# Kernel tuning notes

Hardware: AMD Instinct MI355X
Metric: run time of the kernel (lower is better)

The kernel has to match this reference:

```python
import jax, jax.numpy as jnp
import numpy as np

N = 100000   # nodes
E = 1000000  # edges
D = 128      # hidden dim (all n_hidden entries)
ED = 21      # edge_dim hard-coded in the module


def setup_inputs() -> dict:
    key = jax.random.key(0)
    ks = jax.random.split(key, 32)
    w = lambda k, shape: (jax.random.normal(k, shape, dtype=jnp.float32) * 0.05)
    inp = {
        "G": jax.random.normal(ks[0], (N, D), dtype=jnp.float32),
        "edge_index": jax.random.randint(ks[1], (2, E), 0, N),
        "edge_attribute": jax.random.normal(ks[2], (E, ED), dtype=jnp.float32),
        # 3-layer node embedding MLP (stacked since all dims are D)
        "emb_W": w(ks[3], (3, D, D)), "emb_b": w(ks[4], (3, D)),
        # 2 ResGatedGraphConv layers (conv3 is unused in forward)
        "key_W": w(ks[5], (2, D, D)), "key_b": w(ks[6], (2, D)),
        "qry_W": w(ks[7], (2, D, D)), "qry_b": w(ks[8], (2, D)),
        "val_W": w(ks[9], (2, D, D)), "val_b": w(ks[10], (2, D)),
        "skp_W": w(ks[11], (2, D, D)), "skp_b": w(ks[12], (2, D)),
        "edg_W": w(ks[13], (2, ED, D)), "edg_b": w(ks[14], (2, D)),
        # graph linears
        "g1_W": w(ks[15], (D, D)), "g1_b": w(ks[16], (D,)),
        "g2_W": w(ks[17], (D, D)), "g2_b": w(ks[18], (D,)),
        # head: concat(node, graph_mean) -> 2D -> D -> D -> 1
        "h1_W": w(ks[19], (2 * D, D)), "h1_b": w(ks[20], (D,)),
        "h2_W": w(ks[21], (D, D)), "h2_b": w(ks[22], (D,)),
        "h3_W": w(ks[23], (D, 1)), "h3_b": w(ks[24], (1,)),
    }
    return inp


def reference(G, edge_index, edge_attribute,
              emb_W, emb_b, key_W, key_b, qry_W, qry_b, val_W, val_b,
              skp_W, skp_b, edg_W, edg_b,
              g1_W, g1_b, g2_W, g2_b, h1_W, h1_b, h2_W, h2_b, h3_W, h3_b):
    x = G
    # embedding MLP: Linear -> ReLU x3
    for i in range(3):
        x = jax.nn.relu(x @ emb_W[i] + emb_b[i])
    src, dst = edge_index[0], edge_index[1]
    # ResGatedGraphConv (PyG): out_i = W_skip x_i + sum_j sigmoid(k_i + q_j + W_e e_ij) * v_j
    for i in range(2):
        k = x @ key_W[i] + key_b[i]   # per target node i
        q = x @ qry_W[i] + qry_b[i]   # per source node j
        v = x @ val_W[i] + val_b[i]
        eta = jax.nn.sigmoid(k[dst] + q[src] + edge_attribute @ edg_W[i] + edg_b[i])  # [E, D]
        agg = jax.ops.segment_sum(eta * v[src], dst, num_segments=N)  # scatter-add [N, D]
        x = jax.nn.relu(agg + x @ skp_W[i] + skp_b[i])
    x = jax.nn.relu(x @ g1_W + g1_b)
    x = x @ g2_W + g2_b
    # per-node concat with mean-pooled graph embedding (vectorized form of the Python loop)
    gmean = jnp.mean(x, axis=0)
    u = jnp.concatenate([x, jnp.broadcast_to(gmean, x.shape)], axis=-1)  # [N, 2D]
    u = jax.nn.relu(u @ h1_W + h1_b)
    u = jax.nn.relu(u @ h2_W + h2_b)
    return u @ h3_W + h3_b  # [N, 1]
```

## Files before the change

kernel.cpp:

```cpp
#include <hip/hip_runtime.h>
#include <hip/hip_bf16.h>

#define DD 128
#define LW 136

typedef __attribute__((ext_vector_type(8))) short bf16x8;
typedef __attribute__((ext_vector_type(4))) float f32x4;

__device__ __forceinline__ void cvt8(const float4 a0, const float4 a1,
                                     bf16x8& hi, bf16x8& lo)
{
    float af[8] = {a0.x, a0.y, a0.z, a0.w, a1.x, a1.y, a1.z, a1.w};
    union { unsigned int u[4]; bf16x8 v; } H, L;
    #pragma unroll
    for (int i = 0; i < 4; ++i) {
        unsigned int b0 = __float_as_uint(af[2*i]);
        unsigned int b1 = __float_as_uint(af[2*i+1]);
        unsigned int h0 = b0 & 0xFFFF0000u;
        unsigned int h1 = b1 & 0xFFFF0000u;
        H.u[i] = (h0 >> 16) | h1;
        float r0 = af[2*i]   - __uint_as_float(h0);
        float r1 = af[2*i+1] - __uint_as_float(h1);
        L.u[i] = (__float_as_uint(r0) >> 16) | (__float_as_uint(r1) & 0xFFFF0000u);
    }
    hi = H.v; lo = L.v;
}

__device__ __forceinline__ float fsig(float z)
{
    return __builtin_amdgcn_rcpf(1.f + __expf(-z));
}

__device__ __forceinline__ void mfma_step(
    const unsigned short* __restrict__ WH, const unsigned short* __restrict__ WL,
    int wavecol, int l15, int kb,
    const bf16x8 ah[4], const bf16x8 al[4], f32x4 acc[4][2])
{
    bf16x8 bh[2], bl[2];
    #pragma unroll
    for (int ni = 0; ni < 2; ++ni) {
        int m = wavecol + ni * 16 + l15;
        bh[ni] = *(const bf16x8*)(WH + (size_t)m * DD + kb);
        bl[ni] = *(const bf16x8*)(WL + (size_t)m * DD + kb);
    }
    #pragma unroll
    for (int mi = 0; mi < 4; ++mi)
        #pragma unroll
        for (int ni = 0; ni < 2; ++ni) {
            acc[mi][ni] = __builtin_amdgcn_mfma_f32_16x16x32_bf16(ah[mi], bh[ni], acc[mi][ni], 0, 0, 0);
            acc[mi][ni] = __builtin_amdgcn_mfma_f32_16x16x32_bf16(ah[mi], bl[ni], acc[mi][ni], 0, 0, 0);
            acc[mi][ni] = __builtin_amdgcn_mfma_f32_16x16x32_bf16(al[mi], bh[ni], acc[mi][ni], 0, 0, 0);
        }
}

__device__ __forceinline__ void glb_layer(
    const float* __restrict__ X, int ldX, const int arow[4],
    const unsigned short* __restrict__ WU,
    int wavecol, int l15, int kg, f32x4 acc[4][2])
{
    const unsigned short* WH = WU;
    const unsigned short* WL = WU + 16384;
    #pragma unroll
    for (int kc = 0; kc < 4; ++kc) {
        const int kb = kc * 32 + kg;
        bf16x8 ah[4], al[4];
        #pragma unroll
        for (int mi = 0; mi < 4; ++mi) {
            const float* p = X + (size_t)arow[mi] * ldX + kb;
            float4 a0 = *(const float4*)p;
            float4 a1 = *(const float4*)(p + 4);
            cvt8(a0, a1, ah[mi], al[mi]);
        }
        mfma_step(WH, WL, wavecol, l15, kb, ah, al, acc);
    }
}

__device__ __forceinline__ void lds_layer(
    const unsigned short (*AH)[LW], const unsigned short (*AL)[LW],
    const unsigned short* __restrict__ WU,
    int wavecol, int l15, int kg, f32x4 acc[4][2])
{
    const unsigned short* WH = WU;
    const unsigned short* WL = WU + 16384;
    #pragma unroll
    for (int kc = 0; kc < 4; ++kc) {
        const int kb = kc * 32 + kg;
        bf16x8 ah[4], al[4];
        #pragma unroll
        for (int mi = 0; mi < 4; ++mi) {
            ah[mi] = *(const bf16x8*)&AH[mi * 16 + l15][kb];
            al[mi] = *(const bf16x8*)&AL[mi * 16 + l15][kb];
        }
        mfma_step(WH, WL, wavecol, l15, kb, ah, al, acc);
    }
}

__device__ __forceinline__ void epi_lds(
    const f32x4 acc[4][2], unsigned short (*AH)[LW], unsigned short (*AL)[LW],
    const float* __restrict__ bias, int wavecol, int l15, int rg, int relu)
{
    #pragma unroll
    for (int ni = 0; ni < 2; ++ni) {
        const int col = wavecol + ni * 16 + l15;
        const float bv = bias[col];
        #pragma unroll
        for (int mi = 0; mi < 4; ++mi)
            #pragma unroll
            for (int r = 0; r < 4; ++r) {
                const int row = mi * 16 + rg + r;
                float v = acc[mi][ni][r] + bv;
                if (relu) v = fmaxf(v, 0.f);
                unsigned int u = __float_as_uint(v), h = u & 0xFFFF0000u;
                float res = v - __uint_as_float(h);
                AH[row][col] = (unsigned short)(h >> 16);
                AL[row][col] = (unsigned short)(__float_as_uint(res) >> 16);
            }
    }
}

__global__ __launch_bounds__(256) void fused_emb3q(
    const float* __restrict__ G, const unsigned short* __restrict__ Wt,
    const float* __restrict__ embb, const float* __restrict__ biasCat,
    float* __restrict__ bfused, int N)
{
    __shared__ unsigned short AH[64][LW], AL[64][LW];
    const int lane = threadIdx.x & 63, wid = threadIdx.x >> 6;
    const int wavecol = wid * 32;
    const int l15 = lane & 15, kg = (lane >> 4) * 8, rg = (lane >> 4) * 4;
    const int row0 = blockIdx.x * 64;

    int arow[4];
    #pragma unroll
    for (int mi = 0; mi < 4; ++mi) {
        int r = row0 + mi * 16 + l15;
        arow[mi] = r < N ? r : N - 1;
    }

    f32x4 acc[4][2] = {};
    glb_layer(G, DD, arow, Wt, wavecol, l15, kg, acc);
    epi_lds(acc, AH, AL, embb, wavecol, l15, rg, 1);
    __syncthreads();

    #pragma unroll
    for (int mi = 0; mi < 4; ++mi)
        #pragma unroll
        for (int ni = 0; ni < 2; ++ni) acc[mi][ni] = (f32x4){0,0,0,0};
    lds_layer(AH, AL, Wt + 32768, wavecol, l15, kg, acc);
    __syncthreads();
    epi_lds(acc, AH, AL, embb + 128, wavecol, l15, rg, 1);
    __syncthreads();

    #pragma unroll
    for (int mi = 0; mi < 4; ++mi)
        #pragma unroll
        for (int ni = 0; ni < 2; ++ni) acc[mi][ni] = (f32x4){0,0,0,0};
    lds_layer(AH, AL, Wt + 65536, wavecol, l15, kg, acc);
    __syncthreads();
    epi_lds(acc, AH, AL, embb + 256, wavecol, l15, rg, 1);
    __syncthreads();

    for (int cb = 0; cb < 4; ++cb) {
        #pragma unroll
        for (int mi = 0; mi < 4; ++mi)
            #pragma unroll
            for (int ni = 0; ni < 2; ++ni) acc[mi][ni] = (f32x4){0,0,0,0};
        lds_layer(AH, AL, Wt + (size_t)(3 + cb) * 32768, wavecol, l15, kg, acc);
        #pragma unroll
        for (int ni = 0; ni < 2; ++ni) {
            const int gcol = cb * 128 + wavecol + ni * 16 + l15;
            const float bv = biasCat[gcol];
            #pragma unroll
            for (int mi = 0; mi < 4; ++mi)
                #pragma unroll
                for (int r = 0; r < 4; ++r) {
                    int row = row0 + mi * 16 + rg + r;
                    if (row < N)
                        bfused[(size_t)row * 512 + gcol] = acc[mi][ni][r] + bv;
                }
        }
    }
}

__global__ __launch_bounds__(256) void fused_kqvs(
    float* __restrict__ bfused, const unsigned short* __restrict__ Wt,
    const float* __restrict__ biasCat, int N)
{
    __shared__ unsigned short AH[64][LW], AL[64][LW];
    const int tid = threadIdx.x;
    const int lane = tid & 63, wid = tid >> 6;
    const int wavecol = wid * 32;
    const int l15 = lane & 15, kg = (lane >> 4) * 8, rg = (lane >> 4) * 4;
    const int row0 = blockIdx.x * 64;

    for (int idx = tid; idx < 64 * 128; idx += 256) {
        const int row = idx >> 7, col = idx & 127;
        int gr = row0 + row; if (gr >= N) gr = N - 1;
        float v = bfused[(size_t)gr * 512 + col];
        unsigned int u = __float_as_uint(v), h = u & 0xFFFF0000u;
        float res = v - __uint_as_float(h);
        AH[row][col] = (unsigned short)(h >> 16);
        AL[row][col] = (unsigned short)(__float_as_uint(res) >> 16);
    }
    __syncthreads();

    f32x4 acc[4][2];
    for (int cb = 0; cb < 4; ++cb) {
        #pragma unroll
        for (int mi = 0; mi < 4; ++mi)
            #pragma unroll
            for (int ni = 0; ni < 2; ++ni) acc[mi][ni] = (f32x4){0,0,0,0};
        lds_layer(AH, AL, Wt + (size_t)cb * 32768, wavecol, l15, kg, acc);
        #pragma unroll
        for (int ni = 0; ni < 2; ++ni) {
            const int gcol = cb * 128 + wavecol + ni * 16 + l15;
            const float bv = biasCat[gcol];
            #pragma unroll
            for (int mi = 0; mi < 4; ++mi)
                #pragma unroll
                for (int r = 0; r < 4; ++r) {
                    int row = row0 + mi * 16 + rg + r;
                    if (row < N)
                        bfused[(size_t)row * 512 + gcol] = acc[mi][ni][r] + bv;
                }
        }
    }
}

__global__ __launch_bounds__(256) void fused_g12(
    float* __restrict__ bfused, const unsigned short* __restrict__ Wt,
    const float* __restrict__ g1b, const float* __restrict__ g2b,
    float* __restrict__ gsum, int N)
{
    __shared__ unsigned short AH[64][LW], AL[64][LW];
    __shared__ float csum[128];
    const int tid = threadIdx.x;
    const int lane = tid & 63, wid = tid >> 6;
    const int wavecol = wid * 32;
    const int l15 = lane & 15, kg = (lane >> 4) * 8, rg = (lane >> 4) * 4;
    const int row0 = blockIdx.x * 64;

    if (tid < 128) csum[tid] = 0.f;

    int arow[4];
    #pragma unroll
    for (int mi = 0; mi < 4; ++mi) {
        int r = row0 + mi * 16 + l15;
        arow[mi] = r < N ? r : N - 1;
    }

    f32x4 acc[4][2] = {};
    glb_layer(bfused, 512, arow, Wt, wavecol, l15, kg, acc);
    epi_lds(acc, AH, AL, g1b, wavecol, l15, rg, 1);
    __syncthreads();

    #pragma unroll
    for (int mi = 0; mi < 4; ++mi)
        #pragma unroll
        for (int ni = 0; ni < 2; ++ni) acc[mi][ni] = (f32x4){0,0,0,0};
    lds_layer(AH, AL, Wt + 32768, wavecol, l15, kg, acc);

    #pragma unroll
    for (int ni = 0; ni < 2; ++ni) {
        const int col = wavecol + ni * 16 + l15;
        const float bv = g2b[col];
        float part = 0.f;
        #pragma unroll
        for (int mi = 0; mi < 4; ++mi)
            #pragma unroll
            for (int r = 0; r < 4; ++r) {
                int row = row0 + mi * 16 + rg + r;
                if (row < N) {
                    float v = acc[mi][ni][r] + bv;
                    bfused[(size_t)row * 512 + 128 + col] = v;
                    part += v;
                }
            }
        atomicAdd(&csum[col], part);
    }
    __syncthreads();
    if (tid < 128) atomicAdd(&gsum[tid], csum[tid]);
}

__global__ __launch_bounds__(256) void fused_head(
    const float* __restrict__ bfused, const unsigned short* __restrict__ Wt,
    const float* __restrict__ cvec, const float* __restrict__ h2b,
    const float* __restrict__ h3w, const float* __restrict__ h3b,
    float* __restrict__ out, int N)
{
    __shared__ unsigned short AH[64][LW], AL[64][LW];
    const int tid = threadIdx.x;
    const int lane = tid & 63, wid = tid >> 6;
    const int wavecol = wid * 32;
    const int l15 = lane & 15, kg = (lane >> 4) * 8, rg = (lane >> 4) * 4;
    const int row0 = blockIdx.x * 64;

    int arow[4];
    #pragma unroll
    for (int mi = 0; mi < 4; ++mi) {
        int r = row0 + mi * 16 + l15;
        arow[mi] = r < N ? r : N - 1;
    }

    f32x4 acc[4][2] = {};
    glb_layer(bfused + 128, 512, arow, Wt, wavecol, l15, kg, acc);
    epi_lds(acc, AH, AL, cvec, wavecol, l15, rg, 1);
    __syncthreads();

    #pragma unroll
    for (int mi = 0; mi < 4; ++mi)
        #pragma unroll
        for (int ni = 0; ni < 2; ++ni) acc[mi][ni] = (f32x4){0,0,0,0};
    lds_layer(AH, AL, Wt + 32768, wavecol, l15, kg, acc);
    __syncthreads();
    epi_lds(acc, AH, AL, h2b, wavecol, l15, rg, 1);
    __syncthreads();

    const int row = tid >> 2, seg = tid & 3;
    float s = 0.f;
    #pragma unroll 8
    for (int j = 0; j < 32; ++j) {
        int col = seg * 32 + j;
        float xv = __uint_as_float((unsigned int)AH[row][col] << 16)
                 + __uint_as_float((unsigned int)AL[row][col] << 16);
        s = fmaf(xv, h3w[col], s);
    }
    s += __shfl_xor(s, 1, 64);
    s += __shfl_xor(s, 2, 64);
    if (seg == 0 && row0 + row < N) out[row0 + row] = s + h3b[0];
}

__global__ __launch_bounds__(256) void prep_weights(
    const float* __restrict__ embW, const float* __restrict__ keyW,
    const float* __restrict__ qryW, const float* __restrict__ valW,
    const float* __restrict__ skpW, const float* __restrict__ g1W,
    const float* __restrict__ g2W, const float* __restrict__ h1W,
    const float* __restrict__ h2W,
    const float* __restrict__ keyb, const float* __restrict__ qryb,
    const float* __restrict__ valb, const float* __restrict__ skpb,
    unsigned short* __restrict__ Wt, float* __restrict__ biasCat)
{
    const int u = blockIdx.x;
    const int t = threadIdx.x;
    __shared__ float T[128][129];

    const float* src;
    if (u < 3)       src = embW + (size_t)u * 16384;
    else if (u < 7)  { const float* p[4] = {keyW, qryW, valW, skpW}; src = p[u - 3]; }
    else if (u < 11) { const float* p[4] = {keyW, qryW, valW, skpW}; src = p[u - 7] + 16384; }
    else if (u == 11) src = g1W;
    else if (u == 12) src = g2W;
    else if (u == 13) src = h1W;
    else              src = h2W;

    #pragma unroll
    for (int i = 0; i < 64; ++i) {
        int idx = t + 256 * i;
        T[idx >> 7][idx & 127] = src[idx];
    }
    __syncthreads();

    unsigned short* dH = Wt + (size_t)u * 32768;
    unsigned short* dL = dH + 16384;
    const int m = t >> 1, kbase = (t & 1) * 64;
    for (int j = 0; j < 64; ++j) {
        int k = kbase + j;
        float a = T[k][m];
        unsigned int b = __float_as_uint(a);
        unsigned int h = b & 0xFFFF0000u;
        float r = a - __uint_as_float(h);
        dH[m * 128 + k] = (unsigned short)(h >> 16);
        dL[m * 128 + k] = (unsigned short)(__float_as_uint(r) >> 16);
    }

    if (u == 0) {
        for (int x = t; x < 1024; x += 256) {
            int L = x >> 9, c = x & 511;
            const float* bp = (c < 128) ? keyb : (c < 256) ? qryb : (c < 384) ? valb : skpb;
            biasCat[x] = bp[L * 128 + (c & 127)];
        }
    }
}

__global__ void hist_kernel(const int* __restrict__ dstA, int* __restrict__ hist, int E)
{
    for (int e = blockIdx.x * blockDim.x + threadIdx.x; e < E;
         e += gridDim.x * blockDim.x)
        atomicAdd(&hist[dstA[e]], 1);
}

__global__ __launch_bounds__(256) void scan1_kernel(
    const int* __restrict__ in, int n_in,
    int* __restrict__ out, int* __restrict__ bsum, int n)
{
    __shared__ int wtot[4];
    const int t = threadIdx.x, lane = t & 63, wv = t >> 6;
    const int base = blockIdx.x * 1024 + t * 4;
    int v[4]; int sum = 0;
    #pragma unroll
    for (int j = 0; j < 4; ++j) {
        int idx = base + j;
        v[j] = (idx < n_in) ? in[idx] : 0;
        sum += v[j];
    }
    int incl = sum;
    #pragma unroll
    for (int d = 1; d < 64; d <<= 1) {
        int y = __shfl_up(incl, d, 64);
        if (lane >= d) incl += y;
    }
    if (lane == 63) wtot[wv] = incl;
    __syncthreads();
    int woff = 0;
    for (int w = 0; w < wv; ++w) woff += wtot[w];
    int run = woff + incl - sum;
    #pragma unroll
    for (int j = 0; j < 4; ++j) {
        int idx = base + j;
        if (idx < n) out[idx] = run;
        run += v[j];
    }
    if (t == 0)
        bsum[blockIdx.x] = wtot[0] + wtot[1] + wtot[2] + wtot[3];
}

__global__ void scan2_kernel(int* __restrict__ bsum, int nb)
{
    if (blockIdx.x == 0 && threadIdx.x == 0) {
        int run = 0;
        for (int i = 0; i < nb; ++i) { int t = bsum[i]; bsum[i] = run; run += t; }
    }
}

__global__ __launch_bounds__(256) void scan3_kernel(
    int* __restrict__ out, const int* __restrict__ bsum,
    int* __restrict__ cursor, int n, int n_nodes)
{
    const int base = blockIdx.x * 1024 + threadIdx.x * 4;
    const int add = bsum[blockIdx.x];
    #pragma unroll
    for (int j = 0; j < 4; ++j) {
        int idx = base + j;
        if (idx < n) {
            int vv = out[idx] + add;
            out[idx] = vv;
            if (idx < n_nodes) cursor[idx] = vv;
        }
    }
}

__global__ void scatter_ea(const int* __restrict__ srcA, const int* __restrict__ dstA,
                           const float* __restrict__ ea, int* __restrict__ cursor,
                           int* __restrict__ srcp, float* __restrict__ eaP, int E)
{
    for (int e = blockIdx.x * blockDim.x + threadIdx.x; e < E;
         e += gridDim.x * blockDim.x) {
        int d = dstA[e];
        int pos = atomicAdd(&cursor[d], 1);
        srcp[pos] = srcA[e];
        const float* s = ea + (size_t)e * 21;
        float* q = eaP + (size_t)pos * 24;
        #pragma unroll
        for (int j = 0; j < 21; ++j) q[j] = s[j];
    }
}

__global__ __launch_bounds__(256) void edge_agg16(
    const int* __restrict__ row_ptr, const int* __restrict__ srcp,
    const float* __restrict__ eaP,
    const float* __restrict__ We, const float* __restrict__ be,
    float* __restrict__ fused, int N)
{
    const int wv = threadIdx.x >> 6, lane = threadIdx.x & 63;
    const int c = lane * 2;

    float2 w[21];
    #pragma unroll
    for (int j = 0; j < 21; ++j)
        w[j] = *(const float2*)(We + j * DD + c);
    const float2 b2 = *(const float2*)(be + c);

    const int dstride = gridDim.x * 4;

    for (int d = blockIdx.x * 4 + wv; d < N; d += dstride) {
        const float2 kd = *(const float2*)(fused + (size_t)d * 512 + c);
        const float2 sk = *(const float2*)(fused + (size_t)d * 512 + 384 + c);

        float ax = 0.f, ay = 0.f;
        const int i0 = __builtin_amdgcn_readfirstlane(row_ptr[d]);
        const int i1 = __builtin_amdgcn_readfirstlane(row_ptr[d + 1]);

        for (int i = i0; i < i1; i += 2) {
            const int iA = i;
            const int iB = (i + 1 < i1) ? i + 1 : i1 - 1;
            const float wgtB = (i + 1 < i1) ? 1.f : 0.f;

            const int sA = __builtin_amdgcn_readfirstlane(srcp[iA]);
            const int sB = __builtin_amdgcn_readfirstlane(srcp[iB]);

            const float* eA = eaP + (size_t)iA * 24;
            const float* eB = eaP + (size_t)iB * 24;
            float aA[21], aB[21];
            #pragma unroll
            for (int j = 0; j < 21; ++j) { aA[j] = eA[j]; aB[j] = eB[j]; }

            const float* fpA = fused + (size_t)sA * 512;
            const float* fpB = fused + (size_t)sB * 512;
            float2 qA = *(const float2*)(fpA + 128 + c);
            float2 vA = *(const float2*)(fpA + 256 + c);
            float2 qB = *(const float2*)(fpB + 128 + c);
            float2 vB = *(const float2*)(fpB + 256 + c);

            float pxA[4] = {0,0,0,0}, pyA[4] = {0,0,0,0};
            float pxB[4] = {0,0,0,0}, pyB[4] = {0,0,0,0};
            #pragma unroll
            for (int j = 0; j < 21; ++j) {
                int s = j & 3;
                pxA[s] = fmaf(aA[j], w[j].x, pxA[s]);
                pyA[s] = fmaf(aA[j], w[j].y, pyA[s]);
                pxB[s] = fmaf(aB[j], w[j].x, pxB[s]);
                pyB[s] = fmaf(aB[j], w[j].y, pyB[s]);
            }
            float exA = (pxA[0] + pxA[1]) + (pxA[2] + pxA[3]) + b2.x;
            float eyA = (pyA[0] + pyA[1]) + (pyA[2] + pyA[3]) + b2.y;
            float exB = (pxB[0] + pxB[1]) + (pxB[2] + pxB[3]) + b2.x;
            float eyB = (pyB[0] + pyB[1]) + (pyB[2] + pyB[3]) + b2.y;

            float gxA = fsig(kd.x + qA.x + exA);
            float gyA = fsig(kd.y + qA.y + eyA);
            float gxB = wgtB * fsig(kd.x + qB.x + exB);
            float gyB = wgtB * fsig(kd.y + qB.y + eyB);

            ax = fmaf(gxA, vA.x, ax);
            ay = fmaf(gyA, vA.y, ay);
            ax = fmaf(gxB, vB.x, ax);
            ay = fmaf(gyB, vB.y, ay);
        }

        float* xr = fused + (size_t)d * 512;
        xr[c]     = fmaxf(ax + sk.x, 0.f);
        xr[c + 1] = fmaxf(ay + sk.y, 0.f);
    }
}

__global__ void cvec_kernel(const float* __restrict__ gsum, const float* __restrict__ h1W,
                            const float* __restrict__ h1b, float* __restrict__ cvec, float invN)
{
    const int m = threadIdx.x;
    float acc = h1b[m];
    for (int k = 0; k < 128; ++k)
        acc = fmaf(gsum[k] * invN, h1W[(size_t)(128 + k) * DD + m], acc);
    cvec[m] = acc;
}

extern "C" void kernel_launch(void* const* d_in, const int* in_sizes, int n_in,
                              void* d_out, int out_size, void* d_ws, size_t ws_size,
                              hipStream_t stream)
{
    const float* G    = (const float*)d_in[0];
    const int*   ei   = (const int*)  d_in[1];
    const float* ea   = (const float*)d_in[2];
    const float* embW = (const float*)d_in[3];
    const float* embb = (const float*)d_in[4];
    const float* keyW = (const float*)d_in[5];
    const float* keyb = (const float*)d_in[6];
    const float* qryW = (const float*)d_in[7];
    const float* qryb = (const float*)d_in[8];
    const float* valW = (const float*)d_in[9];
    const float* valb = (const float*)d_in[10];
    const float* skpW = (const float*)d_in[11];
    const float* skpb = (const float*)d_in[12];
    const float* edgW = (const float*)d_in[13];
    const float* edgb = (const float*)d_in[14];
    const float* g1W  = (const float*)d_in[15];
    const float* g1b  = (const float*)d_in[16];
    const float* g2W  = (const float*)d_in[17];
    const float* g2b  = (const float*)d_in[18];
    const float* h1W  = (const float*)d_in[19];
    const float* h1b  = (const float*)d_in[20];
    const float* h2W  = (const float*)d_in[21];
    const float* h2b  = (const float*)d_in[22];
    const float* h3W  = (const float*)d_in[23];
    const float* h3b  = (const float*)d_in[24];

    const int N = in_sizes[0] / DD;
    const int E = in_sizes[2] / 21;
    const int* srcA = ei;
    const int* dstA = ei + E;

    float* bfused = (float*)d_ws;
    float* gsum   = bfused + (size_t)N * 512;
    float* cvec   = gsum + DD;
    float* biasCat= cvec + DD;
    unsigned short* Wt = (unsigned short*)(biasCat + 1024);
    int* hist = (int*)((char*)Wt + (size_t)15 * 32768 * 2);
    int* row  = hist + N;
    int* cur  = row + N + 1;
    int* bsum = cur + N;
    int* srcp = bsum + 128;
    float* eaP = (float*)(srcp + E);

    const int fgrid   = (N + 63) / 64;
    const int aggGrid = 2048;
    const int nScan = N + 1;
    const int nb = (nScan + 1023) / 1024;

    prep_weights<<<15, 256, 0, stream>>>(embW, keyW, qryW, valW, skpW,
                                         g1W, g2W, h1W, h2W,
                                         keyb, qryb, valb, skpb, Wt, biasCat);
    hipMemsetAsync(hist, 0, (size_t)N * sizeof(int), stream);
    hipMemsetAsync(gsum, 0, DD * sizeof(float), stream);
    hist_kernel<<<1024, 256, 0, stream>>>(dstA, hist, E);
    scan1_kernel<<<nb, 256, 0, stream>>>(hist, N, row, bsum, nScan);
    scan2_kernel<<<1, 64, 0, stream>>>(bsum, nb);
    scan3_kernel<<<nb, 256, 0, stream>>>(row, bsum, cur, nScan, N);
    scatter_ea<<<1024, 256, 0, stream>>>(srcA, dstA, ea, cur, srcp, eaP, E);

    #define UNIT(u) (Wt + (size_t)(u) * 32768)

    fused_emb3q<<<fgrid, 256, 0, stream>>>(G, Wt, embb, biasCat, bfused, N);

    edge_agg16<<<aggGrid, 256, 0, stream>>>(row, srcp, eaP,
                                            edgW + 0, edgb + 0, bfused, N);

    fused_kqvs<<<fgrid, 256, 0, stream>>>(bfused, UNIT(7), biasCat + 512, N);
    edge_agg16<<<aggGrid, 256, 0, stream>>>(row, srcp, eaP,
                                            edgW + 21*DD, edgb + DD, bfused, N);

    fused_g12<<<fgrid, 256, 0, stream>>>(bfused, UNIT(11), g1b, g2b, gsum, N);

    cvec_kernel<<<1, DD, 0, stream>>>(gsum, h1W, h1b, cvec, 1.0f / (float)N);

    fused_head<<<fgrid, 256, 0, stream>>>(bfused, UNIT(13), cvec, h2b, h3W, h3b,
                                          (float*)d_out, N);
}
```

Measured before the change: 1.077 ms.

## Process two destination nodes per wavefront with one-shot grid instead of grid-stride

The edge aggregation kernel now assigns two destination nodes to each wavefront and walks their edge lists in lockstep, so the two independent gathers per iteration come from different nodes instead of consecutive edges of one node. The persistent grid-stride loop is replaced by a grid sized to cover all nodes once. This aims to improve memory-level parallelism and remove the odd-degree padding waste of the old pairing. The cost is imbalance when the two nodes' degrees differ, since the loop runs to the larger degree with masked work, and it pays the per-block weight load many more times.

```diff
diff --git a/kernel.cpp b/kernel.cpp
--- a/kernel.cpp
+++ b/kernel.cpp
@@ -464,13 +464,17 @@
     }
 }
 
-__global__ __launch_bounds__(256) void edge_agg16(
+__global__ __launch_bounds__(256) void edge_agg17(
     const int* __restrict__ row_ptr, const int* __restrict__ srcp,
     const float* __restrict__ eaP,
     const float* __restrict__ We, const float* __restrict__ be,
     float* __restrict__ fused, int N)
 {
     const int wv = threadIdx.x >> 6, lane = threadIdx.x & 63;
+    const int d0 = blockIdx.x * 8 + wv * 2;
+    const int d1 = d0 + 1;
+    if (d0 >= N) return;
+    const bool has1 = d1 < N;
     const int c = lane * 2;
 
     float2 w[21];
@@ -479,66 +483,78 @@
         w[j] = *(const float2*)(We + j * DD + c);
     const float2 b2 = *(const float2*)(be + c);
 
-    const int dstride = gridDim.x * 4;
-
-    for (int d = blockIdx.x * 4 + wv; d < N; d += dstride) {
-        const float2 kd = *(const float2*)(fused + (size_t)d * 512 + c);
-        const float2 sk = *(const float2*)(fused + (size_t)d * 512 + 384 + c);
-
-        float ax = 0.f, ay = 0.f;
-        const int i0 = __builtin_amdgcn_readfirstlane(row_ptr[d]);
-        const int i1 = __builtin_amdgcn_readfirstlane(row_ptr[d + 1]);
-
-        for (int i = i0; i < i1; i += 2) {
-            const int iA = i;
-            const int iB = (i + 1 < i1) ? i + 1 : i1 - 1;
-            const float wgtB = (i + 1 < i1) ? 1.f : 0.f;
-
-            const int sA = __builtin_amdgcn_readfirstlane(srcp[iA]);
-            const int sB = __builtin_amdgcn_readfirstlane(srcp[iB]);
-
-            const float* eA = eaP + (size_t)iA * 24;
-            const float* eB = eaP + (size_t)iB * 24;
-            float aA[21], aB[21];
-            #pragma unroll
-            for (int j = 0; j < 21; ++j) { aA[j] = eA[j]; aB[j] = eB[j]; }
-
-            const float* fpA = fused + (size_t)sA * 512;
-            const float* fpB = fused + (size_t)sB * 512;
-            float2 qA = *(const float2*)(fpA + 128 + c);
-            float2 vA = *(const float2*)(fpA + 256 + c);
-            float2 qB = *(const float2*)(fpB + 128 + c);
-            float2 vB = *(const float2*)(fpB + 256 + c);
-
-            float pxA[4] = {0,0,0,0}, pyA[4] = {0,0,0,0};
-            float pxB[4] = {0,0,0,0}, pyB[4] = {0,0,0,0};
-            #pragma unroll
-            for (int j = 0; j < 21; ++j) {
-                int s = j & 3;
-                pxA[s] = fmaf(aA[j], w[j].x, pxA[s]);
-                pyA[s] = fmaf(aA[j], w[j].y, pyA[s]);
-                pxB[s] = fmaf(aB[j], w[j].x, pxB[s]);
-                pyB[s] = fmaf(aB[j], w[j].y, pyB[s]);
-            }
-            float exA = (pxA[0] + pxA[1]) + (pxA[2] + pxA[3]) + b2.x;
-            float eyA = (pyA[0] + pyA[1]) + (pyA[2] + pyA[3]) + b2.y;
-            float exB = (pxB[0] + pxB[1]) + (pxB[2] + pxB[3]) + b2.x;
-            float eyB = (pyB[0] + pyB[1]) + (pyB[2] + pyB[3]) + b2.y;
-
-            float gxA = fsig(kd.x + qA.x + exA);
-            float gyA = fsig(kd.y + qA.y + eyA);
-            float gxB = wgtB * fsig(kd.x + qB.x + exB);
-            float gyB = wgtB * fsig(kd.y + qB.y + eyB);
-
-            ax = fmaf(gxA, vA.x, ax);
-            ay = fmaf(gyA, vA.y, ay);
-            ax = fmaf(gxB, vB.x, ax);
-            ay = fmaf(gyB, vB.y, ay);
-        }
-
-        float* xr = fused + (size_t)d * 512;
-        xr[c]     = fmaxf(ax + sk.x, 0.f);
-        xr[c + 1] = fmaxf(ay + sk.y, 0.f);
+    const float2 kd0 = *(const float2*)(fused + (size_t)d0 * 512 + c);
+    const float2 sk0 = *(const float2*)(fused + (size_t)d0 * 512 + 384 + c);
+    const float2 kd1 = has1 ? *(const float2*)(fused + (size_t)d1 * 512 + c) : kd0;
+    const float2 sk1 = has1 ? *(const float2*)(fused + (size_t)d1 * 512 + 384 + c) : sk0;
+
+    const int a0 = __builtin_amdgcn_readfirstlane(row_ptr[d0]);
+    const int a1 = __builtin_amdgcn_readfirstlane(row_ptr[d0 + 1]);
+    const int b0 = has1 ? __builtin_amdgcn_readfirstlane(row_ptr[d1]) : 0;
+    const int b1 = has1 ? __builtin_amdgcn_readfirstlane(row_ptr[d1 + 1]) : 0;
+    const int na = a1 - a0;
+    const int nb2 = b1 - b0;
+    const int nmax = na > nb2 ? na : nb2;
+
+    float ax0 = 0.f, ay0 = 0.f, ax1 = 0.f, ay1 = 0.f;
+
+    for (int t = 0; t < nmax; ++t) {
+        const int ta = t < na ? t : (na - 1);
+        const float wA = (t < na) ? 1.f : 0.f;
+        const int iA = a0 + (ta < 0 ? 0 : ta);
+        const int tb = t < nb2 ? t : (nb2 - 1);
+        const float wB = (has1 && t < nb2) ? 1.f : 0.f;
+        const int iB = b0 + (tb < 0 ? 0 : tb);
+
+        const int sA = __builtin_amdgcn_readfirstlane(srcp[iA]);
+        const int sB = __builtin_amdgcn_readfirstlane(srcp[iB]);
+
+        const float* eA = eaP + (size_t)iA * 24;
+        const float* eB = eaP + (size_t)iB * 24;
+        float aA[21], aB[21];
+        #pragma unroll
+        for (int j = 0; j < 21; ++j) { aA[j] = eA[j]; aB[j] = eB[j]; }
+
+        const float* fpA = fused + (size_t)sA * 512;
+        const float* fpB = fused + (size_t)sB * 512;
+        float2 qA = *(const float2*)(fpA + 128 + c);
+        float2 vA = *(const float2*)(fpA + 256 + c);
+        float2 qB = *(const float2*)(fpB + 128 + c);
+        float2 vB = *(const float2*)(fpB + 256 + c);
+
+        float pxA[4] = {0,0,0,0}, pyA[4] = {0,0,0,0};
+        float pxB[4] = {0,0,0,0}, pyB[4] = {0,0,0,0};
+        #pragma unroll
+        for (int j = 0; j < 21; ++j) {
+            int s = j & 3;
+            pxA[s] = fmaf(aA[j], w[j].x, pxA[s]);
+            pyA[s] = fmaf(aA[j], w[j].y, pyA[s]);
+            pxB[s] = fmaf(aB[j], w[j].x, pxB[s]);
+            pyB[s] = fmaf(aB[j], w[j].y, pyB[s]);
+        }
+        float exA = (pxA[0] + pxA[1]) + (pxA[2] + pxA[3]) + b2.x;
+        float eyA = (pyA[0] + pyA[1]) + (pyA[2] + pyA[3]) + b2.y;
+        float exB = (pxB[0] + pxB[1]) + (pxB[2] + pxB[3]) + b2.x;
+        float eyB = (pyB[0] + pyB[1]) + (pyB[2] + pyB[3]) + b2.y;
+
+        float gxA = wA * fsig(kd0.x + qA.x + exA);
+        float gyA = wA * fsig(kd0.y + qA.y + eyA);
+        float gxB = wB * fsig(kd1.x + qB.x + exB);
+        float gyB = wB * fsig(kd1.y + qB.y + eyB);
+
+        ax0 = fmaf(gxA, vA.x, ax0);
+        ay0 = fmaf(gyA, vA.y, ay0);
+        ax1 = fmaf(gxB, vB.x, ax1);
+        ay1 = fmaf(gyB, vB.y, ay1);
+    }
+
+    float* xr0 = fused + (size_t)d0 * 512;
+    xr0[c]     = fmaxf(ax0 + sk0.x, 0.f);
+    xr0[c + 1] = fmaxf(ay0 + sk0.y, 0.f);
+    if (has1) {
+        float* xr1 = fused + (size_t)d1 * 512;
+        xr1[c]     = fmaxf(ax1 + sk1.x, 0.f);
+        xr1[c + 1] = fmaxf(ay1 + sk1.y, 0.f);
     }
 }
 
@@ -600,7 +616,7 @@
     float* eaP = (float*)(srcp + E);
 
     const int fgrid   = (N + 63) / 64;
-    const int aggGrid = 2048;
+    const int aggGrid = (N + 7) / 8;
     const int nScan = N + 1;
     const int nb = (nScan + 1023) / 1024;
 
@@ -619,11 +635,11 @@
 
     fused_emb3q<<<fgrid, 256, 0, stream>>>(G, Wt, embb, biasCat, bfused, N);
 
-    edge_agg16<<<aggGrid, 256, 0, stream>>>(row, srcp, eaP,
+    edge_agg17<<<aggGrid, 256, 0, stream>>>(row, srcp, eaP,
                                             edgW + 0, edgb + 0, bfused, N);
 
     fused_kqvs<<<fgrid, 256, 0, stream>>>(bfused, UNIT(7), biasCat + 512, N);
-    edge_agg16<<<aggGrid, 256, 0, stream>>>(row, srcp, eaP,
+    edge_agg17<<<aggGrid, 256, 0, stream>>>(row, srcp, eaP,
                                             edgW + 21*DD, edgb + DD, bfused, N);
 
     fused_g12<<<fgrid, 256, 0, stream>>>(bfused, UNIT(11), g1b, g2b, gsum, N);
```

Result: slower. 1.180 ms (+9.5%).
